# Kernel optimization log

Measured on AMD Instinct MI355X. Metric: run time of the kernel, lower is better.

Reference implementation:

```python
import jax, jax.numpy as jnp
import numpy as np

TRIANGLE_TABLE = np.array([
    [-1,-1,-1,-1,-1,-1],[1,0,2,-1,-1,-1],[4,0,3,-1,-1,-1],[1,4,2,1,3,4],
    [3,1,5,-1,-1,-1],[2,3,0,2,5,3],[1,4,0,1,5,4],[4,2,5,-1,-1,-1],
    [4,5,2,-1,-1,-1],[4,1,0,4,5,1],[3,2,0,3,5,2],[1,3,5,-1,-1,-1],
    [4,1,2,4,3,1],[3,0,4,-1,-1,-1],[2,0,1,-1,-1,-1],[-1,-1,-1,-1,-1,-1]], dtype=np.int64)
NUM_TRIANGLES_TABLE = np.array([0,1,1,2,1,2,2,1,1,2,2,1,2,1,1,0], dtype=np.int64)
BASE_TET_EDGES = np.array([0,1,0,2,0,3,1,2,1,3,2,3], dtype=np.int64)


def _topology(sdf_np, tet_np):
    """Integer/no-grad part of marching tets (matches torch.no_grad block)."""
    occ = sdf_np > 0                                   # [N]
    occ_f4 = occ[tet_np]                               # [F,4]
    occ_sum = occ_f4.sum(-1)
    valid = (occ_sum > 0) & (occ_sum < 4)              # surface-crossing tets
    tets = tet_np[valid]                               # [T,4]
    edges = tets[:, BASE_TET_EDGES].reshape(-1, 2)     # [T*6,2]
    edges = np.sort(edges, axis=1)                     # canonical (min,max) == sort_edges
    unique_edges, idx_map = np.unique(edges, axis=0, return_inverse=True)
    idx_map = idx_map.reshape(-1)
    mask_edges = occ[unique_edges].sum(-1) == 1        # edges crossing the surface
    mapping = np.full(unique_edges.shape[0], -1, dtype=np.int64)
    mapping[mask_edges] = np.arange(int(mask_edges.sum()), dtype=np.int64)
    idx_map = mapping[idx_map].reshape(-1, 6)          # per-tet edge->vert ids
    interp_v = unique_edges[mask_edges]                # [M,2] endpoints to interpolate
    v_id = 1 << np.arange(4, dtype=np.int64)
    tetindex = (occ_f4[valid].astype(np.int64) * v_id).sum(-1)   # [T] case index 0..15
    num_tri = NUM_TRIANGLES_TABLE[tetindex]
    tt = TRIANGLE_TABLE[tetindex]
    faces1 = np.take_along_axis(idx_map[num_tri == 1], tt[num_tri == 1][:, :3], axis=1).reshape(-1, 3)
    faces2 = np.take_along_axis(idx_map[num_tri == 2], tt[num_tri == 2][:, :6], axis=1).reshape(-1, 3)
    faces = np.concatenate([faces1, faces2], axis=0)
    return interp_v, faces


def setup_inputs() -> dict:
    key = jax.random.key(0)
    k1, k2, k3 = jax.random.split(key, 3)
    N, F = 300000, 1500000
    pos_nx3 = jax.random.normal(k1, (N, 3), dtype=jnp.float32)
    sdf_n = jax.random.normal(k2, (N,), dtype=jnp.float32)
    tet_fx4 = jax.random.randint(k3, (F, 4), 0, N, dtype=jnp.int64)
    return {"pos_nx3": pos_nx3, "sdf_n": sdf_n, "tet_fx4": tet_fx4}


def reference(pos_nx3, sdf_n, tet_fx4):
    # topology (index-valued, non-differentiable) computed on host
    interp_v, faces = _topology(np.asarray(sdf_n), np.asarray(tet_fx4))
    iv = jnp.asarray(interp_v)                         # [M,2]
    ep = pos_nx3[iv]                                   # [M,2,3] endpoint positions
    es = sdf_n[iv] * jnp.array([1.0, -1.0], dtype=sdf_n.dtype)  # [M,2] = (a, -b)
    denom = es.sum(axis=1, keepdims=True)              # a - b
    w = es[:, ::-1] / denom                            # flip: (-b, a)/(a-b)
    verts = (ep * w[..., None]).sum(axis=1)            # linear interpolation at sdf=0
    return verts, jnp.asarray(faces)
```

## Files before the change

### kernel.cpp

```cpp
#include <hip/hip_runtime.h>
#include <stdint.h>

static __device__ __constant__ int d_TRI[16][6] = {
  {-1,-1,-1,-1,-1,-1},{1,0,2,-1,-1,-1},{4,0,3,-1,-1,-1},{1,4,2,1,3,4},
  {3,1,5,-1,-1,-1},{2,3,0,2,5,3},{1,4,0,1,5,4},{4,2,5,-1,-1,-1},
  {4,5,2,-1,-1,-1},{4,1,0,4,5,1},{3,2,0,3,5,2},{1,3,5,-1,-1,-1},
  {4,1,2,4,3,1},{3,0,4,-1,-1,-1},{2,0,1,-1,-1,-1},{-1,-1,-1,-1,-1,-1}};
static __device__ __constant__ int d_NT[16] = {0,1,1,2,1,2,2,1,1,2,2,1,2,1,1,0};
static __device__ __constant__ int d_EA[6] = {0,0,0,1,1,2};
static __device__ __constant__ int d_EB[6] = {1,2,3,2,3,3};

#define SB 256
#define SI 8
#define STILE (SB*SI)

__global__ void k_scan_partial(const unsigned* __restrict__ in, unsigned* __restrict__ bsum, int n) {
  int b = blockIdx.x;
  int base = b * STILE;
  __shared__ unsigned sh[SB];
  unsigned s = 0;
  for (int i = threadIdx.x; i < STILE; i += SB) {
    int idx = base + i;
    s += (idx < n) ? in[idx] : 0u;
  }
  sh[threadIdx.x] = s; __syncthreads();
  for (int st = SB/2; st > 0; st >>= 1) {
    if (threadIdx.x < st) sh[threadIdx.x] += sh[threadIdx.x + st];
    __syncthreads();
  }
  if (threadIdx.x == 0) bsum[b] = sh[0];
}

__global__ void k_scan_mid(const unsigned* __restrict__ bsum, unsigned* __restrict__ boff,
                           int B, unsigned* __restrict__ total_dst) {
  int t = threadIdx.x;
  unsigned loc[SI];
  int base = t * SI;
  unsigned s = 0;
  #pragma unroll
  for (int i = 0; i < SI; ++i) {
    int idx = base + i;
    unsigned v = (idx < B) ? bsum[idx] : 0u;
    loc[i] = s; s += v;
  }
  __shared__ unsigned sh[SB];
  sh[t] = s; __syncthreads();
  for (int o = 1; o < SB; o <<= 1) {
    unsigned v = (t >= o) ? sh[t - o] : 0u;
    __syncthreads();
    sh[t] += v;
    __syncthreads();
  }
  unsigned texcl = sh[t] - s;
  #pragma unroll
  for (int i = 0; i < SI; ++i) {
    int idx = base + i;
    if (idx < B) boff[idx] = texcl + loc[i];
  }
  if (t == SB - 1 && total_dst) *total_dst = sh[SB - 1];
}

__global__ void k_scan_final(const unsigned* __restrict__ in, const unsigned* __restrict__ boff,
                             unsigned* __restrict__ out, int n) {
  int b = blockIdx.x;
  int base = b * STILE + threadIdx.x * SI;
  unsigned loc[SI];
  unsigned s = 0;
  #pragma unroll
  for (int i = 0; i < SI; ++i) {
    int idx = base + i;
    unsigned v = (idx < n) ? in[idx] : 0u;
    loc[i] = s; s += v;
  }
  __shared__ unsigned sh[SB];
  int t = threadIdx.x;
  sh[t] = s; __syncthreads();
  for (int o = 1; o < SB; o <<= 1) {
    unsigned v = (t >= o) ? sh[t - o] : 0u;
    __syncthreads();
    sh[t] += v;
    __syncthreads();
  }
  unsigned texcl = sh[t] - s;
  unsigned bo = boff[b];
  #pragma unroll
  for (int i = 0; i < SI; ++i) {
    int idx = base + i;
    if (idx < n) out[idx] = bo + texcl + loc[i];
  }
}

__global__ void k_copy_u32(unsigned* __restrict__ dst, const unsigned* __restrict__ src, int n) {
  int i = blockIdx.x * blockDim.x + threadIdx.x;
  if (i < n) dst[i] = src[i];
}

__global__ void k_classify(const int* __restrict__ tet, const float* __restrict__ sdf,
                           unsigned* __restrict__ cnt, unsigned* __restrict__ t1,
                           unsigned* __restrict__ t2, int F) {
  int f = blockIdx.x * blockDim.x + threadIdx.x;
  if (f >= F) return;
  int4 q = reinterpret_cast<const int4*>(tet)[f];
  int v[4] = {q.x, q.y, q.z, q.w};
  int oc[4];
  #pragma unroll
  for (int i = 0; i < 4; ++i) oc[i] = sdf[v[i]] > 0.0f;
  int s = oc[0] + oc[1] + oc[2] + oc[3];
  int valid = (s > 0) & (s < 4);
  int tix = oc[0] | (oc[1] << 1) | (oc[2] << 2) | (oc[3] << 3);
  int nt = valid ? d_NT[tix] : 0;
  t1[f] = (nt == 1) ? 1u : 0u;
  t2[f] = (nt == 2) ? 1u : 0u;
  if (!valid) return;
  #pragma unroll
  for (int e = 0; e < 6; ++e) {
    int a = v[d_EA[e]], b = v[d_EB[e]];
    if (oc[d_EA[e]] != oc[d_EB[e]]) {
      int lo = a < b ? a : b;
      atomicAdd(&cnt[lo], 1u);
    }
  }
}

__global__ void k_scatter(const int* __restrict__ tet, const float* __restrict__ sdf,
                          unsigned* __restrict__ cursor, unsigned* __restrict__ inst, int F) {
  int f = blockIdx.x * blockDim.x + threadIdx.x;
  if (f >= F) return;
  int4 q = reinterpret_cast<const int4*>(tet)[f];
  int v[4] = {q.x, q.y, q.z, q.w};
  int oc[4];
  #pragma unroll
  for (int i = 0; i < 4; ++i) oc[i] = sdf[v[i]] > 0.0f;
  int s = oc[0] + oc[1] + oc[2] + oc[3];
  if (s == 0 || s == 4) return;
  #pragma unroll
  for (int e = 0; e < 6; ++e) {
    int a = v[d_EA[e]], b = v[d_EB[e]];
    if (oc[d_EA[e]] != oc[d_EB[e]]) {
      int lo = a < b ? a : b;
      int hi = a < b ? b : a;
      unsigned p = atomicAdd(&cursor[lo], 1u);
      inst[p] = (unsigned)hi;
    }
  }
}

#define SORT_CAP 2048
__global__ void k_sortdedupe(const unsigned* __restrict__ off, unsigned* __restrict__ inst,
                             unsigned* __restrict__ uniqtmp, unsigned* __restrict__ ucnt, int N) {
  int v0 = blockIdx.x;
  if (v0 >= N) return;
  unsigned base = off[v0];
  unsigned n = off[v0 + 1] - base;
  if (n == 0) { if (threadIdx.x == 0) ucnt[v0] = 0u; return; }
  __shared__ unsigned sv[SORT_CAP];
  if (n <= SORT_CAP) {
    for (unsigned k = threadIdx.x; k < n; k += 64) sv[k] = inst[base + k];
    __syncthreads();
    for (unsigned k = threadIdx.x; k < n; k += 64) {
      unsigned val = sv[k];
      unsigned r = 0;
      for (unsigned j = 0; j < n; ++j) {
        unsigned w = sv[j];
        r += (w < val) || (w == val && j < k);
      }
      uniqtmp[base + r] = val;
    }
  } else {
    for (unsigned k = threadIdx.x; k < n; k += 64) {
      unsigned val = inst[base + k];
      unsigned r = 0;
      for (unsigned j = 0; j < n; ++j) {
        unsigned w = inst[base + j];
        r += (w < val) || (w == val && j < k);
      }
      uniqtmp[base + r] = val;
    }
  }
  __syncthreads();
  if (threadIdx.x == 0) {
    unsigned u = 0, prev = 0xFFFFFFFFu;
    for (unsigned k = 0; k < n; ++k) {
      unsigned val = uniqtmp[base + k];
      if (k == 0 || val != prev) { inst[base + u++] = val; prev = val; }
    }
    ucnt[v0] = u;
  }
}

__global__ void k_verts(const unsigned* __restrict__ off, const unsigned* __restrict__ uoff,
                        const unsigned* __restrict__ ucnt, const unsigned* __restrict__ inst,
                        unsigned* __restrict__ uniq, const float* __restrict__ pos,
                        const float* __restrict__ sdf, float* __restrict__ out, int N) {
  int v0 = blockIdx.x;
  if (v0 >= N) return;
  unsigned u = ucnt[v0];
  if (u == 0) return;
  unsigned base = off[v0], ub = uoff[v0];
  float a = sdf[v0];
  float p0x = pos[3 * (size_t)v0 + 0], p0y = pos[3 * (size_t)v0 + 1], p0z = pos[3 * (size_t)v0 + 2];
  for (unsigned k = threadIdx.x; k < u; k += 64) {
    unsigned v1 = inst[base + k];
    unsigned r = ub + k;
    uniq[r] = v1;
    float b = sdf[v1];
    float d = a - b;
    float w0 = -b / d;
    float w1 = a / d;
    size_t ro = (size_t)3 * r;
    out[ro + 0] = p0x * w0 + pos[3 * (size_t)v1 + 0] * w1;
    out[ro + 1] = p0y * w0 + pos[3 * (size_t)v1 + 1] * w1;
    out[ro + 2] = p0z * w0 + pos[3 * (size_t)v1 + 2] * w1;
  }
}

__global__ void k_faces(const int* __restrict__ tet, const float* __restrict__ sdf,
                        const unsigned* __restrict__ uoff, const unsigned* __restrict__ ucnt,
                        const unsigned* __restrict__ uniq, const unsigned* __restrict__ P1,
                        const unsigned* __restrict__ P2, float* __restrict__ out, int F, int N) {
  int f = blockIdx.x * blockDim.x + threadIdx.x;
  if (f >= F) return;
  int4 q = reinterpret_cast<const int4*>(tet)[f];
  int v[4] = {q.x, q.y, q.z, q.w};
  int oc[4];
  #pragma unroll
  for (int i = 0; i < 4; ++i) oc[i] = sdf[v[i]] > 0.0f;
  int s = oc[0] + oc[1] + oc[2] + oc[3];
  if (s == 0 || s == 4) return;
  int tix = oc[0] | (oc[1] << 1) | (oc[2] << 2) | (oc[3] << 3);
  int nt = d_NT[tix];
  int rank[6];
  #pragma unroll
  for (int e = 0; e < 6; ++e) {
    int a = v[d_EA[e]], b = v[d_EB[e]];
    if (oc[d_EA[e]] != oc[d_EB[e]]) {
      int lo = a < b ? a : b;
      int hi = a < b ? b : a;
      unsigned lbase = uoff[lo];
      unsigned len = ucnt[lo];
      unsigned loI = 0, hiI = len;
      while (loI < hiI) {
        unsigned mid = (loI + hiI) >> 1;
        if ((int)uniq[lbase + mid] < hi) loI = mid + 1; else hiI = mid;
      }
      rank[e] = (int)(lbase + loI);
    } else {
      rank[e] = -1;
    }
  }
  unsigned M = uoff[N];
  float* fo = out + (size_t)3 * M;
  const int* tt = d_TRI[tix];
  if (nt == 1) {
    unsigned r = P1[f];
    size_t o = (size_t)3 * r;
    fo[o + 0] = (float)rank[tt[0]];
    fo[o + 1] = (float)rank[tt[1]];
    fo[o + 2] = (float)rank[tt[2]];
  } else {
    unsigned T1 = P1[F];
    unsigned r0 = T1 + 2u * P2[f];
    size_t o = (size_t)3 * r0;
    #pragma unroll
    for (int c = 0; c < 6; ++c) fo[o + c] = (float)rank[tt[c]];
  }
}

static void run_scan(const unsigned* in, unsigned* out, int n,
                     unsigned* bsum, unsigned* boff, hipStream_t s) {
  int B = (n + STILE - 1) / STILE;
  k_scan_partial<<<B, SB, 0, s>>>(in, bsum, n);
  k_scan_mid<<<1, SB, 0, s>>>(bsum, boff, B, out + n);
  k_scan_final<<<B, SB, 0, s>>>(in, boff, out, n);
}

extern "C" void kernel_launch(void* const* d_in, const int* in_sizes, int n_in,
                              void* d_out, int out_size, void* d_ws, size_t ws_size,
                              hipStream_t stream) {
  const float* pos = (const float*)d_in[0];
  const float* sdf = (const float*)d_in[1];
  const int* tet = (const int*)d_in[2];
  int N = in_sizes[1];
  int F = in_sizes[2] / 4;
  float* out = (float*)d_out;

  char* w = (char*)d_ws;
  size_t o = 0;
  auto take = [&](size_t bytes) -> char* {
    char* p = w + o;
    o = (o + bytes + 255) & ~(size_t)255;
    return p;
  };
  unsigned* cnt    = (unsigned*)take((size_t)(N + 1) * 4);
  unsigned* off    = (unsigned*)take((size_t)(N + 1) * 4);
  unsigned* cursor = (unsigned*)take((size_t)(N + 1) * 4);
  unsigned* ucnt   = (unsigned*)take((size_t)(N + 1) * 4);
  unsigned* uoff   = (unsigned*)take((size_t)(N + 1) * 4);
  unsigned* t1     = (unsigned*)take((size_t)(F + 1) * 4);
  unsigned* P1     = (unsigned*)take((size_t)(F + 1) * 4);
  unsigned* t2     = (unsigned*)take((size_t)(F + 1) * 4);
  unsigned* P2     = (unsigned*)take((size_t)(F + 1) * 4);
  unsigned* inst   = (unsigned*)take((size_t)4 * F * 4);
  unsigned* uniq   = (unsigned*)take((size_t)4 * F * 4);
  unsigned* bsum   = (unsigned*)take(4096 * 4);
  unsigned* boff   = (unsigned*)take(4096 * 4);

  int TB = 256;
  int FB = (F + TB - 1) / TB;

  hipMemsetAsync(cnt, 0, (size_t)N * 4, stream);
  k_classify<<<FB, TB, 0, stream>>>(tet, sdf, cnt, t1, t2, F);
  run_scan(cnt, off, N, bsum, boff, stream);
  k_copy_u32<<<(N + TB - 1) / TB, TB, 0, stream>>>(cursor, off, N);
  k_scatter<<<FB, TB, 0, stream>>>(tet, sdf, cursor, inst, F);
  k_sortdedupe<<<N, 64, 0, stream>>>(off, inst, uniq, ucnt, N);
  run_scan(ucnt, uoff, N, bsum, boff, stream);
  k_verts<<<N, 64, 0, stream>>>(off, uoff, ucnt, inst, uniq, pos, sdf, out, N);
  run_scan(t1, P1, F, bsum, boff, stream);
  run_scan(t2, P2, F, bsum, boff, stream);
  k_faces<<<FB, TB, 0, stream>>>(tet, sdf, uoff, ucnt, uniq, P1, P2, out, F, N);
}
```

Measured before the change: 1.197 ms.

## Pack four vertices per block, wave-level dedupe, drop cursor copy, merge face scans

Sort/dedupe and vertex kernels now process four vertices per 256-thread block, one wavefront each, replacing block-wide syncs with wave-local LDS waits. The serial single-thread dedupe becomes a ballot/popcount compaction done in shared memory. The cursor copy kernel is removed by advancing the offset array with atomics and recovering each start as off minus cnt. The two face-count scans are merged into one scan over a concatenated array. This cuts launch count, idle threads, and serial work, but the large-list fallback relies on wave-level memory waits for correctness.

```diff
diff --git a/kernel.cpp b/kernel.cpp
--- a/kernel.cpp
+++ b/kernel.cpp
@@ -10,6 +10,17 @@
 static __device__ __constant__ int d_EA[6] = {0,0,0,1,1,2};
 static __device__ __constant__ int d_EB[6] = {1,2,3,2,3,3};
 
+__device__ __forceinline__ void wave_sync_lds() {
+  __builtin_amdgcn_sched_barrier(0);
+  asm volatile("s_waitcnt lgkmcnt(0)" ::: "memory");
+  __builtin_amdgcn_sched_barrier(0);
+}
+__device__ __forceinline__ void wave_sync_vm() {
+  __builtin_amdgcn_sched_barrier(0);
+  asm volatile("s_waitcnt vmcnt(0)" ::: "memory");
+  __builtin_amdgcn_sched_barrier(0);
+}
+
 #define SB 256
 #define SI 8
 #define STILE (SB*SI)
@@ -90,14 +101,9 @@
   }
 }
 
-__global__ void k_copy_u32(unsigned* __restrict__ dst, const unsigned* __restrict__ src, int n) {
-  int i = blockIdx.x * blockDim.x + threadIdx.x;
-  if (i < n) dst[i] = src[i];
-}
 
 __global__ void k_classify(const int* __restrict__ tet, const float* __restrict__ sdf,
-                           unsigned* __restrict__ cnt, unsigned* __restrict__ t1,
-                           unsigned* __restrict__ t2, int F) {
+                           unsigned* __restrict__ cnt, unsigned* __restrict__ t12, int F) {
   int f = blockIdx.x * blockDim.x + threadIdx.x;
   if (f >= F) return;
   int4 q = reinterpret_cast<const int4*>(tet)[f];
@@ -109,8 +115,8 @@
   int valid = (s > 0) & (s < 4);
   int tix = oc[0] | (oc[1] << 1) | (oc[2] << 2) | (oc[3] << 3);
   int nt = valid ? d_NT[tix] : 0;
-  t1[f] = (nt == 1) ? 1u : 0u;
-  t2[f] = (nt == 2) ? 1u : 0u;
+  t12[f] = (nt == 1) ? 1u : 0u;
+  t12[F + f] = (nt == 2) ? 1u : 0u;
   if (!valid) return;
   #pragma unroll
   for (int e = 0; e < 6; ++e) {
@@ -123,7 +129,7 @@
 }
 
 __global__ void k_scatter(const int* __restrict__ tet, const float* __restrict__ sdf,
-                          unsigned* __restrict__ cursor, unsigned* __restrict__ inst, int F) {
+                          unsigned* __restrict__ off, unsigned* __restrict__ inst, int F) {
   int f = blockIdx.x * blockDim.x + threadIdx.x;
   if (f >= F) return;
   int4 q = reinterpret_cast<const int4*>(tet)[f];
@@ -139,67 +145,92 @@
     if (oc[d_EA[e]] != oc[d_EB[e]]) {
       int lo = a < b ? a : b;
       int hi = a < b ? b : a;
-      unsigned p = atomicAdd(&cursor[lo], 1u);
+      unsigned p = atomicAdd(&off[lo], 1u);
       inst[p] = (unsigned)hi;
     }
   }
 }
 
-#define SORT_CAP 2048
-__global__ void k_sortdedupe(const unsigned* __restrict__ off, unsigned* __restrict__ inst,
-                             unsigned* __restrict__ uniqtmp, unsigned* __restrict__ ucnt, int N) {
-  int v0 = blockIdx.x;
+#define CAP 512
+__global__ void k_sortdedupe(const unsigned* __restrict__ off, const unsigned* __restrict__ cnt,
+                             unsigned* __restrict__ inst, unsigned* __restrict__ gtmp,
+                             unsigned* __restrict__ ucnt, int N) {
+  __shared__ unsigned sA[4][CAP];
+  __shared__ unsigned sBv[4][CAP];
+  int w = threadIdx.x >> 6;
+  int lane = threadIdx.x & 63;
+  int v0 = blockIdx.x * 4 + w;
   if (v0 >= N) return;
-  unsigned base = off[v0];
-  unsigned n = off[v0 + 1] - base;
-  if (n == 0) { if (threadIdx.x == 0) ucnt[v0] = 0u; return; }
-  __shared__ unsigned sv[SORT_CAP];
-  if (n <= SORT_CAP) {
-    for (unsigned k = threadIdx.x; k < n; k += 64) sv[k] = inst[base + k];
-    __syncthreads();
-    for (unsigned k = threadIdx.x; k < n; k += 64) {
-      unsigned val = sv[k];
+  unsigned n = cnt[v0];
+  if (n == 0) { if (lane == 0) ucnt[v0] = 0u; return; }
+  unsigned base = off[v0] - n;
+
+  if (n <= CAP) {
+    for (unsigned k = lane; k < n; k += 64) sA[w][k] = inst[base + k];
+    wave_sync_lds();
+    for (unsigned k = lane; k < n; k += 64) {
+      unsigned val = sA[w][k];
       unsigned r = 0;
       for (unsigned j = 0; j < n; ++j) {
-        unsigned w = sv[j];
-        r += (w < val) || (w == val && j < k);
-      }
-      uniqtmp[base + r] = val;
-    }
+        unsigned x = sA[w][j];
+        r += (x < val) || (x == val && j < k);
+      }
+      sBv[w][r] = val;
+    }
+    wave_sync_lds();
+    unsigned ub = 0;
+    for (unsigned c = 0; c < n; c += 64) {
+      unsigned k = c + (unsigned)lane;
+      bool act = k < n;
+      unsigned val = act ? sBv[w][k] : 0u;
+      bool flag = act && (k == 0 || val != sBv[w][k - 1]);
+      unsigned long long m = __ballot((int)flag);
+      if (flag) {
+        unsigned pos = ub + (unsigned)__popcll(m & ((1ull << lane) - 1ull));
+        inst[base + pos] = val;
+      }
+      ub += (unsigned)__popcll(m);
+    }
+    if (lane == 0) ucnt[v0] = ub;
   } else {
-    for (unsigned k = threadIdx.x; k < n; k += 64) {
+    for (unsigned k = lane; k < n; k += 64) {
       unsigned val = inst[base + k];
       unsigned r = 0;
       for (unsigned j = 0; j < n; ++j) {
-        unsigned w = inst[base + j];
-        r += (w < val) || (w == val && j < k);
-      }
-      uniqtmp[base + r] = val;
-    }
-  }
-  __syncthreads();
-  if (threadIdx.x == 0) {
-    unsigned u = 0, prev = 0xFFFFFFFFu;
-    for (unsigned k = 0; k < n; ++k) {
-      unsigned val = uniqtmp[base + k];
-      if (k == 0 || val != prev) { inst[base + u++] = val; prev = val; }
-    }
-    ucnt[v0] = u;
-  }
-}
-
-__global__ void k_verts(const unsigned* __restrict__ off, const unsigned* __restrict__ uoff,
-                        const unsigned* __restrict__ ucnt, const unsigned* __restrict__ inst,
-                        unsigned* __restrict__ uniq, const float* __restrict__ pos,
-                        const float* __restrict__ sdf, float* __restrict__ out, int N) {
-  int v0 = blockIdx.x;
+        unsigned x = inst[base + j];
+        r += (x < val) || (x == val && j < k);
+      }
+      gtmp[base + r] = val;
+    }
+    wave_sync_vm();
+    __threadfence_block();
+    if (lane == 0) {
+      unsigned u = 0, prev = 0xFFFFFFFFu;
+      for (unsigned k = 0; k < n; ++k) {
+        unsigned val = gtmp[base + k];
+        if (k == 0 || val != prev) { inst[base + u++] = val; prev = val; }
+      }
+      ucnt[v0] = u;
+    }
+  }
+}
+
+__global__ void k_verts(const unsigned* __restrict__ off, const unsigned* __restrict__ cnt,
+                        const unsigned* __restrict__ uoff, const unsigned* __restrict__ ucnt,
+                        const unsigned* __restrict__ inst, unsigned* __restrict__ uniq,
+                        const float* __restrict__ pos, const float* __restrict__ sdf,
+                        float* __restrict__ out, int N) {
+  int w = threadIdx.x >> 6;
+  int lane = threadIdx.x & 63;
+  int v0 = blockIdx.x * 4 + w;
   if (v0 >= N) return;
   unsigned u = ucnt[v0];
   if (u == 0) return;
-  unsigned base = off[v0], ub = uoff[v0];
+  unsigned base = off[v0] - cnt[v0];
+  unsigned ub = uoff[v0];
   float a = sdf[v0];
   float p0x = pos[3 * (size_t)v0 + 0], p0y = pos[3 * (size_t)v0 + 1], p0z = pos[3 * (size_t)v0 + 2];
-  for (unsigned k = threadIdx.x; k < u; k += 64) {
+  for (unsigned k = lane; k < u; k += 64) {
     unsigned v1 = inst[base + k];
     unsigned r = ub + k;
     uniq[r] = v1;
@@ -216,8 +247,8 @@
 
 __global__ void k_faces(const int* __restrict__ tet, const float* __restrict__ sdf,
                         const unsigned* __restrict__ uoff, const unsigned* __restrict__ ucnt,
-                        const unsigned* __restrict__ uniq, const unsigned* __restrict__ P1,
-                        const unsigned* __restrict__ P2, float* __restrict__ out, int F, int N) {
+                        const unsigned* __restrict__ uniq, const unsigned* __restrict__ C,
+                        float* __restrict__ out, int F, int N) {
   int f = blockIdx.x * blockDim.x + threadIdx.x;
   if (f >= F) return;
   int4 q = reinterpret_cast<const int4*>(tet)[f];
@@ -252,14 +283,14 @@
   float* fo = out + (size_t)3 * M;
   const int* tt = d_TRI[tix];
   if (nt == 1) {
-    unsigned r = P1[f];
+    unsigned r = C[f];
     size_t o = (size_t)3 * r;
     fo[o + 0] = (float)rank[tt[0]];
     fo[o + 1] = (float)rank[tt[1]];
     fo[o + 2] = (float)rank[tt[2]];
   } else {
-    unsigned T1 = P1[F];
-    unsigned r0 = T1 + 2u * P2[f];
+    unsigned T1 = C[F];
+    unsigned r0 = T1 + 2u * (C[F + f] - T1);
     size_t o = (size_t)3 * r0;
     #pragma unroll
     for (int c = 0; c < 6; ++c) fo[o + c] = (float)rank[tt[c]];
@@ -291,32 +322,28 @@
     o = (o + bytes + 255) & ~(size_t)255;
     return p;
   };
-  unsigned* cnt    = (unsigned*)take((size_t)(N + 1) * 4);
-  unsigned* off    = (unsigned*)take((size_t)(N + 1) * 4);
-  unsigned* cursor = (unsigned*)take((size_t)(N + 1) * 4);
-  unsigned* ucnt   = (unsigned*)take((size_t)(N + 1) * 4);
-  unsigned* uoff   = (unsigned*)take((size_t)(N + 1) * 4);
-  unsigned* t1     = (unsigned*)take((size_t)(F + 1) * 4);
-  unsigned* P1     = (unsigned*)take((size_t)(F + 1) * 4);
-  unsigned* t2     = (unsigned*)take((size_t)(F + 1) * 4);
-  unsigned* P2     = (unsigned*)take((size_t)(F + 1) * 4);
-  unsigned* inst   = (unsigned*)take((size_t)4 * F * 4);
-  unsigned* uniq   = (unsigned*)take((size_t)4 * F * 4);
-  unsigned* bsum   = (unsigned*)take(4096 * 4);
-  unsigned* boff   = (unsigned*)take(4096 * 4);
+  unsigned* cnt  = (unsigned*)take((size_t)(N + 1) * 4);
+  unsigned* off  = (unsigned*)take((size_t)(N + 1) * 4);
+  unsigned* ucnt = (unsigned*)take((size_t)(N + 1) * 4);
+  unsigned* uoff = (unsigned*)take((size_t)(N + 1) * 4);
+  unsigned* t12  = (unsigned*)take((size_t)2 * F * 4);
+  unsigned* C    = (unsigned*)take(((size_t)2 * F + 1) * 4);
+  unsigned* inst = (unsigned*)take((size_t)4 * F * 4);
+  unsigned* uniq = (unsigned*)take((size_t)4 * F * 4);
+  unsigned* bsum = (unsigned*)take(4096 * 4);
+  unsigned* boff = (unsigned*)take(4096 * 4);
 
   int TB = 256;
   int FB = (F + TB - 1) / TB;
+  int NB4 = (N + 3) / 4;
 
   hipMemsetAsync(cnt, 0, (size_t)N * 4, stream);
-  k_classify<<<FB, TB, 0, stream>>>(tet, sdf, cnt, t1, t2, F);
+  k_classify<<<FB, TB, 0, stream>>>(tet, sdf, cnt, t12, F);
   run_scan(cnt, off, N, bsum, boff, stream);
-  k_copy_u32<<<(N + TB - 1) / TB, TB, 0, stream>>>(cursor, off, N);
-  k_scatter<<<FB, TB, 0, stream>>>(tet, sdf, cursor, inst, F);
-  k_sortdedupe<<<N, 64, 0, stream>>>(off, inst, uniq, ucnt, N);
+  k_scatter<<<FB, TB, 0, stream>>>(tet, sdf, off, inst, F);
+  k_sortdedupe<<<NB4, TB, 0, stream>>>(off, cnt, inst, uniq, ucnt, N);
   run_scan(ucnt, uoff, N, bsum, boff, stream);
-  k_verts<<<N, 64, 0, stream>>>(off, uoff, ucnt, inst, uniq, pos, sdf, out, N);
-  run_scan(t1, P1, F, bsum, boff, stream);
-  run_scan(t2, P2, F, bsum, boff, stream);
-  k_faces<<<FB, TB, 0, stream>>>(tet, sdf, uoff, ucnt, uniq, P1, P2, out, F, N);
-}
+  k_verts<<<NB4, TB, 0, stream>>>(off, cnt, uoff, ucnt, inst, uniq, pos, sdf, out, N);
+  run_scan(t12, C, 2 * F, bsum, boff, stream);
+  k_faces<<<FB, TB, 0, stream>>>(tet, sdf, uoff, ucnt, uniq, C, out, F, N);
+}
```

Result: faster. 970.7 us (-18.9%).
